# Kernel tuning notes

Measured on AMD Instinct MI355X. Metric: run time of the kernel, lower is better.

The kernel has to match this reference:

```python
import jax, jax.numpy as jnp
import numpy as np

B, Z, A = 1024, 512, 8          # batch_size, z_dim, action_dim
AH, ZH = 64, 512                # action_hidden_dim, z_hidden_dim
N_NEG = 100                     # n_neg_actions
TEMP = 0.1                      # temperature
TOP_K = (1, 3, 10)


def forward_model(z, a, Wa, ba, W1, b1, W2, b2):
    # MLP forward model with skip connection (z_delta=True):
    # embed action, concat with z, 2-layer MLP predicting a delta.
    h_a = jax.nn.relu(a @ Wa + ba)                                   # [..., AH]
    h = jax.nn.relu(jnp.concatenate([jnp.broadcast_to(z, a.shape[:-1] + (Z,)), h_a], axis=-1) @ W1 + b1)  # [..., ZH]
    delta = h @ W2 + b2                                              # [..., Z]
    return z + delta


def setup_inputs() -> dict:
    key = jax.random.key(0)
    ks = jax.random.split(key, 8)
    def w(k, shape, fan_in):
        return jax.random.normal(k, shape, jnp.float32) / np.float32(np.sqrt(fan_in))
    z = jax.random.normal(ks[0], (B, Z), jnp.float32)
    z_next = jax.random.normal(ks[1], (B, Z), jnp.float32)
    z_next_hat = jax.random.normal(ks[2], (B, Z), jnp.float32)
    actions = jax.random.normal(ks[3], (B, A), jnp.float32)
    Wa = w(ks[4], (A, AH), A)
    ba = jnp.zeros((AH,), jnp.float32)
    W1 = w(ks[5], (Z + AH, ZH), Z + AH)
    b1 = jnp.zeros((ZH,), jnp.float32)
    W2 = w(ks[6], (ZH, Z), ZH)
    b2 = jnp.zeros((Z,), jnp.float32)
    return {"z": z, "z_next": z_next, "z_next_hat": z_next_hat, "actions": actions,
            "Wa": Wa, "ba": ba, "W1": W1, "b1": b1, "W2": W2, "b2": b2}


def reference(z, z_next, z_next_hat, actions, Wa, ba, W1, b1, W2, b2):
    # ControlCPC.compute_loss with dot_product_similarity, vectorized:
    # the Python loop over n_neg_actions rolled-action forward-model calls
    # becomes one batched [n-1, B, ...] forward-model evaluation.
    batch = z.shape[0]
    n = min(N_NEG, batch)
    sim = z_next @ z_next_hat.T                                      # [B, B] positives on diagonal
    shifts = jnp.arange(1, n)
    neg_actions = jax.vmap(lambda i: jnp.roll(actions, -i, axis=0))(shifts)  # [n-1, B, A]
    z_hat_neg = forward_model(z[None], neg_actions, Wa, ba, W1, b1, W2, b2)  # [n-1, B, Z]
    neg_sim = jnp.einsum('nbz,bz->bn', z_hat_neg, z_next)            # diag of similarity per shift
    sim_mat = jnp.concatenate([sim, neg_sim], axis=1)                # [B, B+n-1]
    # INCE loss, positives on diagonal
    logp = jax.nn.log_softmax(sim_mat / jnp.float32(TEMP), axis=1)
    loss = -jnp.mean(jnp.diagonal(logp))                             # diagonal takes first B entries
    labels = jnp.arange(batch)[:, None]
    accs = []
    for k in TOP_K:
        _, preds = jax.lax.top_k(sim_mat, k)                         # [B, k]
        accs.append(jnp.mean((preds == labels).astype(jnp.float32)) * k)
    return (loss, accs[0], accs[1], accs[2])
```

## Files before the change

### kernel.cpp

```cpp
#include <hip/hip_runtime.h>
#include <math.h>

#define B_SZ 1024
#define Z_DIM 512
#define A_DIM 8
#define AH 64
#define ZH 512
#define NNEG 99
#define INV_T 10.0f

typedef __attribute__((ext_vector_type(8))) short short8;
typedef __attribute__((ext_vector_type(4))) float f32x4;

__device__ __forceinline__ short bf16rn(float x) {
    unsigned u = __float_as_uint(x);
    u += 0x7fffu + ((u >> 16) & 1u);
    return (short)(u >> 16);
}
__device__ __forceinline__ void cvt8rn(float4 x0, float4 x1, short8& h) {
    h[0] = bf16rn(x0.x); h[1] = bf16rn(x0.y); h[2] = bf16rn(x0.z); h[3] = bf16rn(x0.w);
    h[4] = bf16rn(x1.x); h[5] = bf16rn(x1.y); h[6] = bf16rn(x1.z); h[7] = bf16rn(x1.w);
}

__device__ __forceinline__ int sw(int m, int kb) { return m * 8 + (kb ^ (m & 7)); }

__global__ __launch_bounds__(256) void prep_kernel(
    const float* __restrict__ W1, const float* __restrict__ actions,
    const float* __restrict__ Wa, const float* __restrict__ ba,
    float* __restrict__ W1T, float* __restrict__ ha, unsigned* __restrict__ cnt)
{
    const int id = blockIdx.x, tid = threadIdx.x;
    if (id == 0 && tid == 0) atomicExch(cnt, 0u);
    if (id < 72) {
        __shared__ float L[64][68];
        int kt = id >> 3, nt = id & 7;
#pragma unroll
        for (int i = 0; i < 4; ++i) {
            int f = tid + i * 256;
            int r = f >> 4, c4 = (f & 15) << 2;
            *(float4*)&L[r][c4] = *(const float4*)&W1[(kt * 64 + r) * 512 + nt * 64 + c4];
        }
        __syncthreads();
#pragma unroll
        for (int i = 0; i < 4; ++i) {
            int f = tid + i * 256;
            int r = f >> 4, c4 = (f & 15) << 2;
            float4 o = {L[c4][r], L[c4 + 1][r], L[c4 + 2][r], L[c4 + 3][r]};
            *(float4*)&W1T[(nt * 64 + r) * 576 + kt * 64 + c4] = o;
        }
    } else if (id < 88) {
        __shared__ float sWa[A_DIM * 64];
        __shared__ float sba[64];
        __shared__ float sact[64][A_DIM];
        int j0 = (id - 72) * 64;
        for (int i = tid; i < A_DIM * 64; i += 256) sWa[i] = Wa[i];
        if (tid < 64) sba[tid] = ba[tid];
        for (int i = tid; i < 64 * A_DIM; i += 256) (&sact[0][0])[i] = actions[j0 * A_DIM + i];
        __syncthreads();
        int r = tid >> 2, c0 = (tid & 3) * 16;
        float o[16];
#pragma unroll
        for (int c = 0; c < 16; ++c) o[c] = sba[c0 + c];
#pragma unroll
        for (int k = 0; k < A_DIM; ++k) {
            float a = sact[r][k];
#pragma unroll
            for (int c = 0; c < 16; ++c) o[c] += a * sWa[k * 64 + c0 + c];
        }
#pragma unroll
        for (int c = 0; c < 16; c += 4) {
            float4 v4 = {fmaxf(o[c], 0.f), fmaxf(o[c + 1], 0.f),
                         fmaxf(o[c + 2], 0.f), fmaxf(o[c + 3], 0.f)};
            *(float4*)&ha[(j0 + r) * 64 + c0 + c] = v4;
        }
    }
}

__global__ __launch_bounds__(256) void mm_kernel(
    const float* __restrict__ z, const float* __restrict__ z_next,
    const float* __restrict__ z_next_hat, const float* __restrict__ W1T,
    const float* __restrict__ b1, const float* __restrict__ W2,
    const float* __restrict__ ha,
    float* __restrict__ sim, float* __restrict__ u, float* __restrict__ v,
    float* __restrict__ g)
{
    __shared__ short Ah[4096], Bh[4096];

    const int id = blockIdx.x;
    const int tid = threadIdx.x;

    const float* Aop; const float* Bop; const float* bias = nullptr;
    float* C; int N, K, lda, ldb, bm0, bn0;
    if (id < 256) {
        int t = id; bn0 = (t & 15) * 64; bm0 = (t >> 4) * 64;
        Aop = z_next; lda = 512; Bop = z_next_hat; ldb = 512;
        C = sim; N = 1024; K = 512;
    } else if (id < 384) {
        int t = id - 256; bn0 = (t & 7) * 64; bm0 = (t >> 3) * 64;
        Aop = z; lda = 512; Bop = W1T; ldb = 576;
        C = u; N = 512; K = 512; bias = b1;
    } else if (id < 512) {
        int t = id - 384; bn0 = (t & 7) * 64; bm0 = (t >> 3) * 64;
        Aop = z_next; lda = 512; Bop = W2; ldb = 512;
        C = v; N = 512; K = 512;
    } else {
        int t = id - 512; bn0 = (t & 7) * 64; bm0 = (t >> 3) * 64;
        Aop = ha; lda = 64; Bop = W1T + 512; ldb = 576;
        C = g; N = 512; K = 64;
    }

    const int lane = tid & 63, wv = tid >> 6;
    const int lm = lane & 15, lq = lane >> 4;
    const int wm = (wv >> 1) * 32, wn = (wv & 1) * 32;
    const int sr = tid >> 2, sq = tid & 3;
    short8* Ah8 = (short8*)Ah; short8* Bh8 = (short8*)Bh;
    f32x4 acc[2][2] = {};

    for (int k0 = 0; k0 < K; k0 += 64) {
        {
            const float* base = &Aop[(bm0 + sr) * lda + k0 + sq * 16];
            float4 x0 = *(const float4*)(base + 0), x1 = *(const float4*)(base + 4);
            float4 x2 = *(const float4*)(base + 8), x3 = *(const float4*)(base + 12);
            short8 h;
            cvt8rn(x0, x1, h); Ah8[sw(sr, 2 * sq)] = h;
            cvt8rn(x2, x3, h); Ah8[sw(sr, 2 * sq + 1)] = h;
        }
        {
            const float* base = &Bop[(bn0 + sr) * ldb + k0 + sq * 16];
            float4 x0 = *(const float4*)(base + 0), x1 = *(const float4*)(base + 4);
            float4 x2 = *(const float4*)(base + 8), x3 = *(const float4*)(base + 12);
            short8 h;
            cvt8rn(x0, x1, h); Bh8[sw(sr, 2 * sq)] = h;
            cvt8rn(x2, x3, h); Bh8[sw(sr, 2 * sq + 1)] = h;
        }
        __syncthreads();
#pragma unroll
        for (int kk = 0; kk < 64; kk += 32) {
            int kbi = (kk >> 3) + lq;
            short8 ah[2], bh[2];
#pragma unroll
            for (int i = 0; i < 2; ++i) {
                ah[i] = Ah8[sw(wm + i * 16 + lm, kbi)];
                bh[i] = Bh8[sw(wn + i * 16 + lm, kbi)];
            }
#pragma unroll
            for (int i = 0; i < 2; ++i)
#pragma unroll
                for (int j = 0; j < 2; ++j)
                    acc[i][j] = __builtin_amdgcn_mfma_f32_16x16x32_bf16(ah[i], bh[j], acc[i][j], 0, 0, 0);
        }
        __syncthreads();
    }
#pragma unroll
    for (int i = 0; i < 2; ++i)
#pragma unroll
        for (int j = 0; j < 2; ++j) {
            int n = bn0 + wn + j * 16 + lm;
            float bb = bias ? bias[n] : 0.0f;
#pragma unroll
            for (int r = 0; r < 4; ++r) {
                int m = bm0 + wm + i * 16 + lq * 4 + r;
                C[m * N + n] = acc[i][j][r] + bb;
            }
        }
}

#define LOADC(GA, GB, kk) { \
    const int q0_ = (kk) * 8; \
    _Pragma("unroll") \
    for (int c_ = 0; c_ < 8; ++c_) { \
        int j_ = (b + 1 + q0_ + c_) & (B_SZ - 1); \
        GA[c_] = *(const float4*)&g[j_ * 512 + lane * 4]; \
        GB[c_] = *(const float4*)&g[j_ * 512 + 256 + lane * 4]; \
    } }

#define LOADC3(GA, GB) { \
    _Pragma("unroll") \
    for (int c_ = 0; c_ < 3; ++c_) { \
        int j_ = (b + 97 + c_) & (B_SZ - 1); \
        GA[c_] = *(const float4*)&g[j_ * 512 + lane * 4]; \
        GB[c_] = *(const float4*)&g[j_ * 512 + 256 + lane * 4]; \
    } }

#define DOTC(T, GA, GB, NC) { \
    _Pragma("unroll") \
    for (int c_ = 0; c_ < (NC); ++c_) { \
        float s_ = 0.0f; \
        s_ += fmaxf(ua.x + GA[c_].x, 0.0f) * va.x; \
        s_ += fmaxf(ua.y + GA[c_].y, 0.0f) * va.y; \
        s_ += fmaxf(ua.z + GA[c_].z, 0.0f) * va.z; \
        s_ += fmaxf(ua.w + GA[c_].w, 0.0f) * va.w; \
        s_ += fmaxf(ub.x + GB[c_].x, 0.0f) * vb.x; \
        s_ += fmaxf(ub.y + GB[c_].y, 0.0f) * vb.y; \
        s_ += fmaxf(ub.z + GB[c_].z, 0.0f) * vb.z; \
        s_ += fmaxf(ub.w + GB[c_].w, 0.0f) * vb.w; \
        T[c_] = s_; \
    } }

#define REDST(T, kk, NC) { \
    for (int off_ = 32; off_; off_ >>= 1) { \
        _Pragma("unroll") \
        for (int c_ = 0; c_ < (NC); ++c_) T[c_] += __shfl_down(T[c_], off_); \
    } \
    if (lane == 0) { \
        _Pragma("unroll") \
        for (int c_ = 0; c_ < (NC); ++c_) rn[(kk) * 8 + c_] = c0 + T[c_]; \
    } }

__global__ __launch_bounds__(256, 2) void row2_kernel(
    const float* __restrict__ sim, const float* __restrict__ u,
    const float* __restrict__ v, const float* __restrict__ g,
    const float* __restrict__ z, const float* __restrict__ z_next,
    const float* __restrict__ b2,
    float* __restrict__ pw, unsigned* __restrict__ cnt, float* __restrict__ out)
{
    const int b = blockIdx.x;
    const int tid = threadIdx.x;
    const int w = tid >> 6, lane = tid & 63;
    __shared__ float rn[104];
    __shared__ float sred[12];
    __shared__ float red[256];
    __shared__ int sdone;

    float4 ua = *(const float4*)&u[b * 512 + lane * 4];
    float4 ub = *(const float4*)&u[b * 512 + 256 + lane * 4];
    float4 va = *(const float4*)&v[b * 512 + lane * 4];
    float4 vb = *(const float4*)&v[b * 512 + 256 + lane * 4];
    float4 s4 = *(const float4*)&sim[b * 1024 + tid * 4];
    float diag = sim[b * 1024 + b];

    float p;
    {
        float4 za = *(const float4*)&z[b * 512 + lane * 4];
        float4 zb = *(const float4*)&z[b * 512 + 256 + lane * 4];
        float4 na = *(const float4*)&z_next[b * 512 + lane * 4];
        float4 nb = *(const float4*)&z_next[b * 512 + 256 + lane * 4];
        float4 ca = *(const float4*)&b2[lane * 4];
        float4 cb = *(const float4*)&b2[256 + lane * 4];
        p  = (za.x + ca.x) * na.x + (za.y + ca.y) * na.y + (za.z + ca.z) * na.z + (za.w + ca.w) * na.w;
        p += (zb.x + cb.x) * nb.x + (zb.y + cb.y) * nb.y + (zb.z + cb.z) * nb.z + (zb.w + cb.w) * nb.w;
    }
    for (int off = 32; off; off >>= 1) p += __shfl_down(p, off);
    const float c0 = __shfl(p, 0);

    {
        const int k0 = w, k1 = w + 4, k2 = w + 8;
        float4 gaA[8], gbA[8], gaB[8], gbB[8];
        float tA[8], tB[8];

        LOADC(gaA, gbA, k0);
        LOADC(gaB, gbB, k1);
        DOTC(tA, gaA, gbA, 8);
        LOADC(gaA, gbA, k2);
        REDST(tA, k0, 8);
        DOTC(tB, gaB, gbB, 8);
        if (w == 0) LOADC3(gaB, gbB);
        REDST(tB, k1, 8);
        DOTC(tA, gaA, gbA, 8);
        REDST(tA, k2, 8);
        if (w == 0) {
            DOTC(tB, gaB, gbB, 3);
            REDST(tB, 12, 3);
        }
    }
    __syncthreads();

    float neg = (tid < NNEG) ? rn[tid] : -3.4e38f;

    float m = fmaxf(fmaxf(s4.x, s4.y), fmaxf(s4.z, s4.w));
    m = fmaxf(m, neg);
    for (int off = 32; off; off >>= 1) m = fmaxf(m, __shfl_xor(m, off));
    if (lane == 0) sred[w] = m;
    __syncthreads();
    m = fmaxf(fmaxf(sred[0], sred[1]), fmaxf(sred[2], sred[3]));

    float es = 0.0f; int ck = 0;
    {
        float xs[4] = {s4.x, s4.y, s4.z, s4.w};
#pragma unroll
        for (int c = 0; c < 4; ++c) {
            int j = tid * 4 + c;
            float x = xs[c];
            es += __expf((x - m) * INV_T);
            if (x > diag) ck++;
            else if (j < b && x == diag) ck++;
        }
    }
    if (tid < NNEG) {
        es += __expf((neg - m) * INV_T);
        if (neg > diag) ck++;
    }
    float ckf = (float)ck;
    for (int off = 32; off; off >>= 1) {
        es += __shfl_down(es, off);
        ckf += __shfl_down(ckf, off);
    }
    if (lane == 0) { sred[4 + w] = es; sred[8 + w] = ckf; }
    __syncthreads();
    if (tid == 0) {
        float est = sred[4] + sred[5] + sred[6] + sred[7];
        int ckt = (int)(sred[8] + sred[9] + sred[10] + sred[11]);
        pw[b * 4 + 0] = (m - diag) * INV_T + logf(est);
        pw[b * 4 + 1] = (ckt < 1) ? 1.0f : 0.0f;
        pw[b * 4 + 2] = (ckt < 3) ? 1.0f : 0.0f;
        pw[b * 4 + 3] = (ckt < 10) ? 1.0f : 0.0f;
        __threadfence();
        unsigned old = atomicAdd(cnt, 1u);
        sdone = (old == 1023u) ? 1 : 0;
    }
    __syncthreads();
    if (sdone) {
        __threadfence();
        int c = tid & 3;
        float s = 0.0f;
        for (int r = tid >> 2; r < 1024; r += 64) s += pw[r * 4 + c];
        red[tid] = s;
        __syncthreads();
        if (tid < 4) {
            float t = 0.0f;
            for (int q = 0; q < 64; ++q) t += red[tid + q * 4];
            out[tid] = t * (1.0f / (float)B_SZ);
        }
    }
}

extern "C" void kernel_launch(void* const* d_in, const int* in_sizes, int n_in,
                              void* d_out, int out_size, void* d_ws, size_t ws_size,
                              hipStream_t stream) {
    const float* z          = (const float*)d_in[0];
    const float* z_next     = (const float*)d_in[1];
    const float* z_next_hat = (const float*)d_in[2];
    const float* actions    = (const float*)d_in[3];
    const float* Wa         = (const float*)d_in[4];
    const float* ba         = (const float*)d_in[5];
    const float* W1         = (const float*)d_in[6];
    const float* b1         = (const float*)d_in[7];
    const float* W2         = (const float*)d_in[8];
    const float* b2         = (const float*)d_in[9];
    float* out = (float*)d_out;

    float* ws   = (float*)d_ws;
    float* sim  = ws;
    float* u    = sim + B_SZ * B_SZ;
    float* v    = u + B_SZ * ZH;
    float* g    = v + B_SZ * ZH;
    float* W1T  = g + B_SZ * ZH;
    float* ha   = W1T + 512 * 576;
    float* pw   = ha + B_SZ * AH;
    unsigned* cnt = (unsigned*)(pw + B_SZ * 4);

    prep_kernel<<<88, 256, 0, stream>>>(W1, actions, Wa, ba, W1T, ha, cnt);
    mm_kernel<<<640, 256, 0, stream>>>(z, z_next, z_next_hat, W1T, b1, W2, ha,
                                       sim, u, v, g);
    row2_kernel<<<1024, 256, 0, stream>>>(sim, u, v, g, z, z_next, b2, pw, cnt, out);
}
```

Baseline: 127.6 us.

## Pre-convert GEMM operands to bf16, use 128x128 tiles with direct global-to-LDS loads

A new conversion kernel turns z, z_next, z_next_hat, W2, the transposed W1 and the action embeddings into bf16 buffers up front. The GEMM kernel then reads bf16 through global_load_lds straight into swizzled shared memory, with 128x128 tiles and a 4x4 MFMA grid per wave. This halves operand bytes, removes the in-loop conversions and raises reuse per tile. In exchange it adds an extra kernel pass and leaves only 160 GEMM blocks. The atomic last-block reduction is also replaced by a separate single-block final kernel, which adds a launch.

```diff
diff --git a/kernel.cpp b/kernel.cpp
--- a/kernel.cpp
+++ b/kernel.cpp
@@ -10,6 +10,7 @@
 #define INV_T 10.0f
 
 typedef __attribute__((ext_vector_type(8))) short short8;
+typedef __attribute__((ext_vector_type(4))) short short4b;
 typedef __attribute__((ext_vector_type(4))) float f32x4;
 
 __device__ __forceinline__ short bf16rn(float x) {
@@ -24,16 +25,41 @@
 
 __device__ __forceinline__ int sw(int m, int kb) { return m * 8 + (kb ^ (m & 7)); }
 
-__global__ __launch_bounds__(256) void prep_kernel(
-    const float* __restrict__ W1, const float* __restrict__ actions,
+#define VMWAIT(N) asm volatile("s_waitcnt vmcnt(" #N ")" ::: "memory")
+__device__ __forceinline__ void raw_barrier() {
+    asm volatile("" ::: "memory");
+    __builtin_amdgcn_s_barrier();
+    asm volatile("" ::: "memory");
+}
+typedef const __attribute__((address_space(1))) void* gas_ptr;
+typedef __attribute__((address_space(3))) void* las_ptr;
+__device__ __forceinline__ void gld_lds16(const void* gsrc, void* ldst) {
+    __builtin_amdgcn_global_load_lds((gas_ptr)gsrc, (las_ptr)ldst, 16, 0, 0);
+}
+
+__global__ __launch_bounds__(256) void cvt_kernel(
+    const float* __restrict__ z, const float* __restrict__ z_next,
+    const float* __restrict__ z_next_hat, const float* __restrict__ W1,
+    const float* __restrict__ W2, const float* __restrict__ actions,
     const float* __restrict__ Wa, const float* __restrict__ ba,
-    float* __restrict__ W1T, float* __restrict__ ha, unsigned* __restrict__ cnt)
+    short* __restrict__ zb, short* __restrict__ znb, short* __restrict__ znhb,
+    short* __restrict__ w1t, short* __restrict__ w2b, short* __restrict__ hab)
 {
     const int id = blockIdx.x, tid = threadIdx.x;
-    if (id == 0 && tid == 0) atomicExch(cnt, 0u);
-    if (id < 72) {
+    if (id < 896) {
+        const float* src; short* dst; int local;
+        if (id < 256)      { src = z;          dst = zb;   local = id; }
+        else if (id < 512) { src = z_next;     dst = znb;  local = id - 256; }
+        else if (id < 768) { src = z_next_hat; dst = znhb; local = id - 512; }
+        else               { src = W2;         dst = w2b;  local = id - 768; }
+        int i8 = local * 2048 + tid * 8;
+        float4 x0 = *(const float4*)&src[i8];
+        float4 x1 = *(const float4*)&src[i8 + 4];
+        short8 h; cvt8rn(x0, x1, h);
+        *(short8*)&dst[i8] = h;
+    } else if (id < 968) {
         __shared__ float L[64][68];
-        int kt = id >> 3, nt = id & 7;
+        int local = id - 896, kt = local >> 3, nt = local & 7;
 #pragma unroll
         for (int i = 0; i < 4; ++i) {
             int f = tid + i * 256;
@@ -45,121 +71,110 @@
         for (int i = 0; i < 4; ++i) {
             int f = tid + i * 256;
             int r = f >> 4, c4 = (f & 15) << 2;
-            float4 o = {L[c4][r], L[c4 + 1][r], L[c4 + 2][r], L[c4 + 3][r]};
-            *(float4*)&W1T[(nt * 64 + r) * 576 + kt * 64 + c4] = o;
-        }
-    } else if (id < 88) {
+            short4b o = {bf16rn(L[c4][r]), bf16rn(L[c4 + 1][r]),
+                         bf16rn(L[c4 + 2][r]), bf16rn(L[c4 + 3][r])};
+            *(short4b*)&w1t[(nt * 64 + r) * 576 + kt * 64 + c4] = o;
+        }
+    } else {
         __shared__ float sWa[A_DIM * 64];
         __shared__ float sba[64];
-        __shared__ float sact[64][A_DIM];
-        int j0 = (id - 72) * 64;
+        int j0 = (id - 968) * 64;
         for (int i = tid; i < A_DIM * 64; i += 256) sWa[i] = Wa[i];
         if (tid < 64) sba[tid] = ba[tid];
-        for (int i = tid; i < 64 * A_DIM; i += 256) (&sact[0][0])[i] = actions[j0 * A_DIM + i];
         __syncthreads();
         int r = tid >> 2, c0 = (tid & 3) * 16;
+        float4 a0 = *(const float4*)&actions[(j0 + r) * A_DIM + 0];
+        float4 a1 = *(const float4*)&actions[(j0 + r) * A_DIM + 4];
+        float av[8] = {a0.x, a0.y, a0.z, a0.w, a1.x, a1.y, a1.z, a1.w};
         float o[16];
 #pragma unroll
         for (int c = 0; c < 16; ++c) o[c] = sba[c0 + c];
 #pragma unroll
-        for (int k = 0; k < A_DIM; ++k) {
-            float a = sact[r][k];
-#pragma unroll
-            for (int c = 0; c < 16; ++c) o[c] += a * sWa[k * 64 + c0 + c];
-        }
+        for (int k = 0; k < A_DIM; ++k)
+#pragma unroll
+            for (int c = 0; c < 16; ++c) o[c] += av[k] * sWa[k * 64 + c0 + c];
 #pragma unroll
         for (int c = 0; c < 16; c += 4) {
-            float4 v4 = {fmaxf(o[c], 0.f), fmaxf(o[c + 1], 0.f),
-                         fmaxf(o[c + 2], 0.f), fmaxf(o[c + 3], 0.f)};
-            *(float4*)&ha[(j0 + r) * 64 + c0 + c] = v4;
-        }
-    }
-}
-
-__global__ __launch_bounds__(256) void mm_kernel(
-    const float* __restrict__ z, const float* __restrict__ z_next,
-    const float* __restrict__ z_next_hat, const float* __restrict__ W1T,
-    const float* __restrict__ b1, const float* __restrict__ W2,
-    const float* __restrict__ ha,
+            short4b h = {bf16rn(fmaxf(o[c], 0.f)),     bf16rn(fmaxf(o[c + 1], 0.f)),
+                         bf16rn(fmaxf(o[c + 2], 0.f)), bf16rn(fmaxf(o[c + 3], 0.f))};
+            *(short4b*)&hab[(j0 + r) * 64 + c0 + c] = h;
+        }
+    }
+}
+
+__global__ __launch_bounds__(256, 2) void mm_kernel(
+    const short* __restrict__ zb, const short* __restrict__ znb,
+    const short* __restrict__ znhb, const short* __restrict__ w1t,
+    const short* __restrict__ w2b, const short* __restrict__ hab,
+    const float* __restrict__ b1,
     float* __restrict__ sim, float* __restrict__ u, float* __restrict__ v,
     float* __restrict__ g)
 {
-    __shared__ short Ah[4096], Bh[4096];
+    __shared__ __align__(16) short Ah[128 * 64], Bh[128 * 64];
 
     const int id = blockIdx.x;
     const int tid = threadIdx.x;
 
-    const float* Aop; const float* Bop; const float* bias = nullptr;
+    const short* A; const short* B; const float* bias = nullptr;
     float* C; int N, K, lda, ldb, bm0, bn0;
-    if (id < 256) {
-        int t = id; bn0 = (t & 15) * 64; bm0 = (t >> 4) * 64;
-        Aop = z_next; lda = 512; Bop = z_next_hat; ldb = 512;
-        C = sim; N = 1024; K = 512;
-    } else if (id < 384) {
-        int t = id - 256; bn0 = (t & 7) * 64; bm0 = (t >> 3) * 64;
-        Aop = z; lda = 512; Bop = W1T; ldb = 576;
-        C = u; N = 512; K = 512; bias = b1;
-    } else if (id < 512) {
-        int t = id - 384; bn0 = (t & 7) * 64; bm0 = (t >> 3) * 64;
-        Aop = z_next; lda = 512; Bop = W2; ldb = 512;
-        C = v; N = 512; K = 512;
+    if (id < 64) {
+        bm0 = (id >> 3) * 128; bn0 = (id & 7) * 128;
+        A = znb; lda = 512; B = znhb; ldb = 512; C = sim; N = 1024; K = 512;
+    } else if (id < 96) {
+        int t = id - 64; bm0 = (t >> 2) * 128; bn0 = (t & 3) * 128;
+        A = zb; lda = 512; B = w1t; ldb = 576; C = u; N = 512; K = 512; bias = b1;
+    } else if (id < 128) {
+        int t = id - 96; bm0 = (t >> 2) * 128; bn0 = (t & 3) * 128;
+        A = znb; lda = 512; B = w2b; ldb = 512; C = v; N = 512; K = 512;
     } else {
-        int t = id - 512; bn0 = (t & 7) * 64; bm0 = (t >> 3) * 64;
-        Aop = ha; lda = 64; Bop = W1T + 512; ldb = 576;
-        C = g; N = 512; K = 64;
+        int t = id - 128; bm0 = (t >> 2) * 128; bn0 = (t & 3) * 128;
+        A = hab; lda = 64; B = w1t + 512; ldb = 576; C = g; N = 512; K = 64;
     }
 
     const int lane = tid & 63, wv = tid >> 6;
     const int lm = lane & 15, lq = lane >> 4;
-    const int wm = (wv >> 1) * 32, wn = (wv & 1) * 32;
-    const int sr = tid >> 2, sq = tid & 3;
-    short8* Ah8 = (short8*)Ah; short8* Bh8 = (short8*)Bh;
-    f32x4 acc[2][2] = {};
+    const int wr = (wv >> 1) * 64, wc = (wv & 1) * 64;
+    short8* A8 = (short8*)Ah; short8* B8 = (short8*)Bh;
+    f32x4 acc[4][4] = {};
 
     for (int k0 = 0; k0 < K; k0 += 64) {
-        {
-            const float* base = &Aop[(bm0 + sr) * lda + k0 + sq * 16];
-            float4 x0 = *(const float4*)(base + 0), x1 = *(const float4*)(base + 4);
-            float4 x2 = *(const float4*)(base + 8), x3 = *(const float4*)(base + 12);
-            short8 h;
-            cvt8rn(x0, x1, h); Ah8[sw(sr, 2 * sq)] = h;
-            cvt8rn(x2, x3, h); Ah8[sw(sr, 2 * sq + 1)] = h;
-        }
-        {
-            const float* base = &Bop[(bn0 + sr) * ldb + k0 + sq * 16];
-            float4 x0 = *(const float4*)(base + 0), x1 = *(const float4*)(base + 4);
-            float4 x2 = *(const float4*)(base + 8), x3 = *(const float4*)(base + 12);
-            short8 h;
-            cvt8rn(x0, x1, h); Bh8[sw(sr, 2 * sq)] = h;
-            cvt8rn(x2, x3, h); Bh8[sw(sr, 2 * sq + 1)] = h;
-        }
-        __syncthreads();
+#pragma unroll
+        for (int q = 0; q < 4; ++q) {
+            int f = q * 256 + tid;
+            int row = f >> 3;
+            int ug = (f & 7) ^ (row & 7);
+            gld_lds16(&A[(bm0 + row) * lda + k0 + ug * 8],
+                      &Ah[(q * 256 + wv * 64) * 8]);
+            gld_lds16(&B[(bn0 + row) * ldb + k0 + ug * 8],
+                      &Bh[(q * 256 + wv * 64) * 8]);
+        }
+        VMWAIT(0);
+        raw_barrier();
 #pragma unroll
         for (int kk = 0; kk < 64; kk += 32) {
             int kbi = (kk >> 3) + lq;
-            short8 ah[2], bh[2];
-#pragma unroll
-            for (int i = 0; i < 2; ++i) {
-                ah[i] = Ah8[sw(wm + i * 16 + lm, kbi)];
-                bh[i] = Bh8[sw(wn + i * 16 + lm, kbi)];
-            }
-#pragma unroll
-            for (int i = 0; i < 2; ++i)
-#pragma unroll
-                for (int j = 0; j < 2; ++j)
+            short8 ah[4], bh[4];
+#pragma unroll
+            for (int i = 0; i < 4; ++i) ah[i] = A8[sw(wr + i * 16 + lm, kbi)];
+#pragma unroll
+            for (int j = 0; j < 4; ++j) bh[j] = B8[sw(wc + j * 16 + lm, kbi)];
+#pragma unroll
+            for (int i = 0; i < 4; ++i)
+#pragma unroll
+                for (int j = 0; j < 4; ++j)
                     acc[i][j] = __builtin_amdgcn_mfma_f32_16x16x32_bf16(ah[i], bh[j], acc[i][j], 0, 0, 0);
         }
-        __syncthreads();
-    }
-#pragma unroll
-    for (int i = 0; i < 2; ++i)
-#pragma unroll
-        for (int j = 0; j < 2; ++j) {
-            int n = bn0 + wn + j * 16 + lm;
+        raw_barrier();
+    }
+#pragma unroll
+    for (int i = 0; i < 4; ++i)
+#pragma unroll
+        for (int j = 0; j < 4; ++j) {
+            int n = bn0 + wc + j * 16 + lm;
             float bb = bias ? bias[n] : 0.0f;
 #pragma unroll
             for (int r = 0; r < 4; ++r) {
-                int m = bm0 + wm + i * 16 + lq * 4 + r;
+                int m = bm0 + wr + i * 16 + lq * 4 + r;
                 C[m * N + n] = acc[i][j][r] + bb;
             }
         }
@@ -212,15 +227,13 @@
     const float* __restrict__ v, const float* __restrict__ g,
     const float* __restrict__ z, const float* __restrict__ z_next,
     const float* __restrict__ b2,
-    float* __restrict__ pw, unsigned* __restrict__ cnt, float* __restrict__ out)
+    float* __restrict__ pw)
 {
     const int b = blockIdx.x;
     const int tid = threadIdx.x;
     const int w = tid >> 6, lane = tid & 63;
     __shared__ float rn[104];
     __shared__ float sred[12];
-    __shared__ float red[256];
-    __shared__ int sdone;
 
     float4 ua = *(const float4*)&u[b * 512 + lane * 4];
     float4 ub = *(const float4*)&u[b * 512 + 256 + lane * 4];
@@ -232,13 +245,13 @@
     float p;
     {
         float4 za = *(const float4*)&z[b * 512 + lane * 4];
-        float4 zb = *(const float4*)&z[b * 512 + 256 + lane * 4];
+        float4 zb4 = *(const float4*)&z[b * 512 + 256 + lane * 4];
         float4 na = *(const float4*)&z_next[b * 512 + lane * 4];
         float4 nb = *(const float4*)&z_next[b * 512 + 256 + lane * 4];
         float4 ca = *(const float4*)&b2[lane * 4];
         float4 cb = *(const float4*)&b2[256 + lane * 4];
         p  = (za.x + ca.x) * na.x + (za.y + ca.y) * na.y + (za.z + ca.z) * na.z + (za.w + ca.w) * na.w;
-        p += (zb.x + cb.x) * nb.x + (zb.y + cb.y) * nb.y + (zb.z + cb.z) * nb.z + (zb.w + cb.w) * nb.w;
+        p += (zb4.x + cb.x) * nb.x + (zb4.y + cb.y) * nb.y + (zb4.z + cb.z) * nb.z + (zb4.w + cb.w) * nb.w;
     }
     for (int off = 32; off; off >>= 1) p += __shfl_down(p, off);
     const float c0 = __shfl(p, 0);
@@ -304,23 +317,23 @@
         pw[b * 4 + 1] = (ckt < 1) ? 1.0f : 0.0f;
         pw[b * 4 + 2] = (ckt < 3) ? 1.0f : 0.0f;
         pw[b * 4 + 3] = (ckt < 10) ? 1.0f : 0.0f;
-        __threadfence();
-        unsigned old = atomicAdd(cnt, 1u);
-        sdone = (old == 1023u) ? 1 : 0;
-    }
+    }
+}
+
+__global__ __launch_bounds__(256) void final_kernel(
+    const float* __restrict__ pw, float* __restrict__ out)
+{
+    __shared__ float red[256];
+    const int tid = threadIdx.x;
+    const int c = tid & 3;
+    float s = 0.0f;
+    for (int r = tid >> 2; r < 1024; r += 64) s += pw[r * 4 + c];
+    red[tid] = s;
     __syncthreads();
-    if (sdone) {
-        __threadfence();
-        int c = tid & 3;
-        float s = 0.0f;
-        for (int r = tid >> 2; r < 1024; r += 64) s += pw[r * 4 + c];
-        red[tid] = s;
-        __syncthreads();
-        if (tid < 4) {
-            float t = 0.0f;
-            for (int q = 0; q < 64; ++q) t += red[tid + q * 4];
-            out[tid] = t * (1.0f / (float)B_SZ);
-        }
+    if (tid < 4) {
+        float t = 0.0f;
+        for (int q = 0; q < 64; ++q) t += red[tid + q * 4];
+        out[tid] = t * (1.0f / (float)B_SZ);
     }
 }
 
@@ -344,13 +357,19 @@
     float* u    = sim + B_SZ * B_SZ;
     float* v    = u + B_SZ * ZH;
     float* g    = v + B_SZ * ZH;
-    float* W1T  = g + B_SZ * ZH;
-    float* ha   = W1T + 512 * 576;
-    float* pw   = ha + B_SZ * AH;
-    unsigned* cnt = (unsigned*)(pw + B_SZ * 4);
-
-    prep_kernel<<<88, 256, 0, stream>>>(W1, actions, Wa, ba, W1T, ha, cnt);
-    mm_kernel<<<640, 256, 0, stream>>>(z, z_next, z_next_hat, W1T, b1, W2, ha,
+    float* pw   = g + B_SZ * ZH;
+    short* zb   = (short*)(pw + B_SZ * 4);
+    short* znb  = zb + B_SZ * Z_DIM;
+    short* znhb = znb + B_SZ * Z_DIM;
+    short* w1t  = znhb + B_SZ * Z_DIM;
+    short* w2b  = w1t + 512 * 576;
+    short* hab  = w2b + 512 * 512;
+
+    cvt_kernel<<<984, 256, 0, stream>>>(z, z_next, z_next_hat, W1, W2,
+                                        actions, Wa, ba,
+                                        zb, znb, znhb, w1t, w2b, hab);
+    mm_kernel<<<160, 256, 0, stream>>>(zb, znb, znhb, w1t, w2b, hab, b1,
                                        sim, u, v, g);
-    row2_kernel<<<1024, 256, 0, stream>>>(sim, u, v, g, z, z_next, b2, pw, cnt, out);
-}
+    row2_kernel<<<1024, 256, 0, stream>>>(sim, u, v, g, z, z_next, b2, pw);
+    final_kernel<<<1, 256, 0, stream>>>(pw, out);
+}
```

After: 115.2 us. 9.7% less time.
